# Performance work log

Measured on AMD Instinct MI355X. Metric: run time of the kernel, lower is better.

Reference implementation:

```python
import jax, jax.numpy as jnp
import numpy as np

BIT = 128
Y_P = 0.5
RIGHT = BIT / 8.0
LEFT = RIGHT / 2.0
UB = BIT / 2.0
ALPHA = 0.1
PCT_NUM, PCT_DEN = 9, 10  # percent = 9/10
C_COEF = (1.0 / RIGHT) * np.log(Y_P / (99.0 * (1.0 - Y_P)))  # slope c (constant since y_p fixed)
A_COEF = -1.0 / (LEFT * C_COEF) * np.log(99.0 * Y_P / (1.0 - Y_P))  # hard-branch factor a
# with y_p=0.5: d = -c*BP, g = -a*c*BP, so f_easy = c*(x-BP), f_hard = a*c*(x-BP)


def setup_inputs() -> dict:
    key = jax.random.key(0)
    k1, k2 = jax.random.split(key)
    N, C = 6144, 200
    u = jax.random.normal(k1, (N, BIT), dtype=jnp.float32)
    labels = jax.random.randint(k2, (N,), 0, C)
    y = jax.nn.one_hot(labels, C, dtype=jnp.int32)
    ind = jnp.arange(N, dtype=jnp.int32)  # unused dataset indices
    return {"u": u, "y": y, "ind": ind}


def reference(u, y, ind):
    sg = jax.lax.stop_gradient
    N = u.shape[0]
    uh = jnp.tanh(u)
    s = (y @ y.T) > 0                      # [N,N] bool similarity (diagonal is True)
    inner = uh @ uh.T                      # [N,N]
    n_sim = s.sum(axis=1)                  # int per-row similar count
    n_dis = N - n_sim
    fn_sim = n_sim.astype(jnp.float32)
    fn_dis = n_dis.astype(jnp.float32)
    idx = jnp.arange(N)[None, :]

    meanS = jnp.clip(jnp.where(s, inner, 0.0).sum(1) / jnp.maximum(fn_sim, 1.0), 0.0, UB)
    meanDS = jnp.clip(jnp.where(s, 0.0, inner).sum(1) / jnp.maximum(fn_dis, 1.0), 0.0, UB)

    dis_sorted = jnp.sort(jnp.where(s, -jnp.inf, inner), axis=1)
    start_dis = (n_dis * PCT_NUM) // PCT_DEN          # int(len*0.9)
    tail_mask = idx >= (N - n_dis + start_dis)[:, None]
    tail_cnt = jnp.maximum((n_dis - start_dis).astype(jnp.float32), 1.0)
    dMax = jnp.clip(jnp.where(tail_mask, dis_sorted, 0.0).sum(1) / tail_cnt, 0.0, UB)

    sim_sorted = jnp.sort(jnp.where(s, inner, jnp.inf), axis=1)
    start_sim = (n_sim * PCT_NUM) // PCT_DEN
    head_mask = idx < (n_sim - start_sim)[:, None]
    head_cnt = jnp.maximum((n_sim - start_sim).astype(jnp.float32), 1.0)
    sMin = jnp.clip(jnp.where(head_mask, sim_sorted, 0.0).sum(1) / head_cnt, 0.0, UB)

    # .item() in the original detaches these -> stop_gradient
    meanS, meanDS, dMax, sMin = map(sg, (meanS, meanDS, dMax, sMin))
    BP = meanS - (UB - meanS) / UB * jnp.abs(meanS - dMax)      # [N]
    BPd = meanDS + meanDS / UB * jnp.abs(meanDS - sMin)         # [N]

    # similar-pair loss: f + log(1+exp(-f)) == softplus(f)
    dc = inner - BP[:, None]
    f_sim = jnp.where(inner > BP[:, None], C_COEF * dc, A_COEF * C_COEF * dc)
    mask_sim = s & (inner != BP[:, None])             # == BP excluded in torch indexing
    cnt_sim = jnp.maximum(mask_sim.sum(1).astype(jnp.float32), 1.0)
    row_pos = jnp.where(mask_sim, jax.nn.softplus(f_sim), 0.0).sum(1) / cnt_sim

    # dissimilar-pair loss: log(1+exp(-f)) == softplus(-f)
    dcd = inner - BPd[:, None]
    f_dis = jnp.where(inner < BPd[:, None], C_COEF * dcd, A_COEF * C_COEF * dcd)
    mask_dis = (~s) & (inner != BPd[:, None])
    cnt_dis = jnp.maximum(mask_dis.sum(1).astype(jnp.float32), 1.0)
    row_neg = jnp.where(mask_dis, jax.nn.softplus(-f_dis), 0.0).sum(1) / cnt_dis

    valid = (n_sim > 0) & (n_dis > 0)
    count = valid.sum().astype(jnp.float32)
    posL = jnp.where(count > 0, jnp.where(valid, row_pos, 0.0).sum() / jnp.maximum(count, 1.0), 0.0)
    navL = jnp.where(count > 0, jnp.where(valid, row_neg, 0.0).sum() / jnp.maximum(count, 1.0), 0.0)

    q_loss = ALPHA * jnp.mean((uh - jnp.sign(uh)) ** 2)
    return posL + navL + q_loss
```

## Files before the change

kernel.cpp:

```cpp
#include <hip/hip_runtime.h>
#include <cstdint>

#define NROW 6144
#define KDIM 128
#define NLAB 200
#define C_COEF (-0.28719499063341177f)
#define UBV 64.0f

typedef _Float16 f16x8 __attribute__((ext_vector_type(8)));
typedef _Float16 f16x2 __attribute__((ext_vector_type(2)));
typedef float f32x4 __attribute__((ext_vector_type(4)));
typedef __attribute__((address_space(1))) const void as1c_void;
typedef __attribute__((address_space(3))) void as3_void;

union U8 { f16x8 h; unsigned u[4]; f16x2 p[4]; };
union CV16 { _Float16 h; unsigned short us; };

__device__ __forceinline__ float softplus_f(float x){
  return fmaxf(x, 0.f) + __logf(1.f + __expf(-fabsf(x)));
}
__device__ __forceinline__ float waveRedF(float v){
#pragma unroll
  for (int o = 32; o; o >>= 1) v += __shfl_down(v, o, 64);
  return v;
}
__device__ __forceinline__ float bfRedF(float v){
#pragma unroll
  for (int o = 32; o; o >>= 1) v += __shfl_xor(v, o, 64);
  return v;
}
__device__ __forceinline__ int bfRedI(int v){
#pragma unroll
  for (int o = 32; o; o >>= 1) v += __shfl_xor(v, o, 64);
  return v;
}
__device__ __forceinline__ int bfMaxI(int v){
#pragma unroll
  for (int o = 32; o; o >>= 1){ int x = __shfl_xor(v, o, 64); v = v > x ? v : x; }
  return v;
}
__device__ __forceinline__ float bfMaxF(float v){
#pragma unroll
  for (int o = 32; o; o >>= 1) v = fmaxf(v, __shfl_xor(v, o, 64));
  return v;
}
__device__ __forceinline__ float val_of_key(unsigned key){
  unsigned bits = (key & 0x8000u) ? (key ^ 0x8000u) : (key ^ 0xFFFFu);
  CV16 cv; cv.us = (unsigned short)bits;
  return (float)cv.h;
}

__global__ __launch_bounds__(256) void k_labtanh(const int* __restrict__ y,
    unsigned char* __restrict__ lab, int* __restrict__ cnt, int* __restrict__ simIdx,
    const float* __restrict__ u, _Float16* __restrict__ uhswz, float* __restrict__ accf){
  const int bid = blockIdx.x;
  const int tid = threadIdx.x;
  const int NLB = NROW / 4;
  if (bid < NLB){
    const int lane = tid & 63;
    const int row = bid * 4 + (tid >> 6);
    if (lane < NLAB / 4){
      const int4 v = ((const int4*)(y + (size_t)row * NLAB))[lane];
      int t = -1;
      if (v.x != 0) t = 4 * lane;
      if (v.y != 0) t = 4 * lane + 1;
      if (v.z != 0) t = 4 * lane + 2;
      if (v.w != 0) t = 4 * lane + 3;
      if (t >= 0){
        lab[row] = (unsigned char)t;
        int p = atomicAdd(&cnt[t], 1);
        if (p < 512) simIdx[t * 512 + p] = row;
      }
    }
    return;
  }
  const int gid = (bid - NLB) * 256 + tid;
  const int row = gid >> 4;
  const int h = gid & 15;
  const int g = h ^ (row & 7);
  const float* sp = u + (size_t)row * KDIM + g * 8;
  float q = 0.f;
  f16x8 o;
#pragma unroll
  for (int t = 0; t < 8; t++){
    float x = sp[t];
    float e2 = __expf(2.f * x);
    float th = 1.f - 2.f * __builtin_amdgcn_rcpf(e2 + 1.f);
    float sg = (th > 0.f) ? 1.f : ((th < 0.f) ? -1.f : 0.f);
    float d = th - sg;
    q += d * d;
    o[t] = (_Float16)th;
  }
  *(f16x8*)(uhswz + (size_t)row * KDIM + h * 8) = o;
  q = waveRedF(q);
  __shared__ float qb[4];
  if ((tid & 63) == 0) qb[tid >> 6] = q;
  __syncthreads();
  if (tid == 0) atomicAdd(&accf[0], qb[0] + qb[1] + qb[2] + qb[3]);
}

__global__ __launch_bounds__(512) void k_mm(const _Float16* __restrict__ A,
    _Float16* __restrict__ out, int row0, int sym){
  int bi, bj;
  if (sym){
    int t = blockIdx.x;
    int b = 0, off = 0;
    while (t >= off + (48 - b)){ off += 48 - b; b++; }
    bi = b; bj = b + (t - off);
  } else {
    bi = blockIdx.y; bj = blockIdx.x;
  }
  __shared__ __align__(16) _Float16 SH[2 * 128 * KDIM];
  const int tid = threadIdx.x;
  const int wav = tid >> 6, lane = tid & 63;
  const bool diag = sym && (bi == bj);

  const char* Ag = (const char*)(A + (size_t)(row0 + bi * 128) * KDIM);
  const char* Bg = (const char*)(A + (size_t)(bj * 128) * KDIM);
  char* Asb = (char*)SH;
  char* Bsb = diag ? Asb : (char*)(SH + 128 * KDIM);
#pragma unroll
  for (int t = 0; t < 4; t++){
    const int ub = wav * 4096 + t * 1024;
    __builtin_amdgcn_global_load_lds((as1c_void*)(Ag + ub + lane * 16),
                                     (as3_void*)(Asb + ub), 16, 0, 0);
    if (!diag)
      __builtin_amdgcn_global_load_lds((as1c_void*)(Bg + ub + lane * 16),
                                       (as3_void*)(Bsb + ub), 16, 0, 0);
  }
  __syncthreads();

  const int quad = lane >> 4, l16 = lane & 15;
  const int wm = (wav >> 2) * 64, wn = (wav & 3) * 32;
  f32x4 acc[4][2];
#pragma unroll
  for (int im = 0; im < 4; im++)
#pragma unroll
    for (int in = 0; in < 2; in++)
      acc[im][in] = (f32x4){0.f, 0.f, 0.f, 0.f};

#pragma unroll
  for (int kb = 0; kb < 4; kb++){
    f16x8 af[4], bf[2];
    const int gidx = kb * 4 + quad;
#pragma unroll
    for (int i = 0; i < 4; i++){
      const int m = wm + i * 16 + l16;
      af[i] = *(const f16x8*)(Asb + m * 256 + ((gidx ^ (m & 7)) << 4));
    }
#pragma unroll
    for (int j = 0; j < 2; j++){
      const int n = wn + j * 16 + l16;
      bf[j] = *(const f16x8*)(Bsb + n * 256 + ((gidx ^ (n & 7)) << 4));
    }
#pragma unroll
    for (int im = 0; im < 4; im++)
#pragma unroll
      for (int in = 0; in < 2; in++)
        acc[im][in] = __builtin_amdgcn_mfma_f32_16x16x32_f16(af[im], bf[in], acc[im][in], 0, 0, 0);
  }
  __syncthreads();

  _Float16* Cs = (_Float16*)SH;
#pragma unroll
  for (int im = 0; im < 4; im++)
#pragma unroll
    for (int in = 0; in < 2; in++)
#pragma unroll
      for (int r = 0; r < 4; r++){
        const int rl = wm + im * 16 + quad * 4 + r;
        const int cl = wn + in * 16 + l16;
        Cs[rl * 132 + cl] = (_Float16)acc[im][in][r];
      }
  __syncthreads();

  _Float16* obase = out + (size_t)(bi * 128) * NROW + (size_t)bj * 128;
  const int s = tid & 15;
  const int rb = tid >> 4;
#pragma unroll
  for (int i = 0; i < 4; i++){
    const int r = rb + i * 32;
    f16x8 vv = *(const f16x8*)(Cs + r * 132 + s * 8);
    *(f16x8*)(obase + (size_t)r * NROW + s * 8) = vv;
  }

  if (sym && bi != bj){
    __syncthreads();
#pragma unroll
    for (int im = 0; im < 4; im++)
#pragma unroll
      for (int in = 0; in < 2; in++)
#pragma unroll
        for (int r = 0; r < 4; r++){
          const int rl = wm + im * 16 + quad * 4 + r;
          const int cl = wn + in * 16 + l16;
          Cs[cl * 132 + rl] = (_Float16)acc[im][in][r];
        }
    __syncthreads();
    _Float16* obase2 = out + (size_t)(bj * 128) * NROW + (size_t)bi * 128;
#pragma unroll
    for (int i = 0; i < 4; i++){
      const int r = rb + i * 32;
      f16x8 vv = *(const f16x8*)(Cs + r * 132 + s * 8);
      *(f16x8*)(obase2 + (size_t)r * NROW + s * 8) = vv;
    }
  }
}

__global__ __launch_bounds__(256) void k_stats(const _Float16* __restrict__ buf,
    const unsigned char* __restrict__ lab, const int* __restrict__ cnt,
    const int* __restrict__ simIdx, float* __restrict__ rowRes, int row0){
  __shared__ int   histS[4][1028];
  __shared__ float simvS[4][512];
  const int tid = threadIdx.x;
  const int lane = tid & 63;
  const int wav = tid >> 6;
  const int lrow = blockIdx.x * 4 + wav;
  const int row = row0 + lrow;
  const int myl = lab[row];
  const int n_sim = cnt[myl];
  const int n_dis = NROW - n_sim;
  if (n_dis == 0 || n_sim == 0) return;
  const int k1 = n_dis - (n_dis * 9) / 10;
  const int k2 = n_sim - (n_sim * 9) / 10;
  const int ns = (n_sim < 512) ? n_sim : 512;

  int*   hist = histS[wav];
  int*   myh  = hist + (lane >> 4) * 257;
  float* simv = simvS[wav];
#pragma unroll
  for (int r = 0; r < 4; r++) *(int4*)&hist[(lane + 64 * r) * 4] = make_int4(0, 0, 0, 0);
  if (lane == 0) *(int4*)&hist[1024] = make_int4(0, 0, 0, 0);

  const f16x8* src = (const f16x8*)(buf + (size_t)lrow * NROW);
  const _Float16* srcs = buf + (size_t)lrow * NROW;

  float sumAll = 0.f;
  const f16x2 ones = (f16x2){(_Float16)1.f, (_Float16)1.f};
#pragma unroll 2
  for (int it = 0; it < 12; ++it){
    U8 x; x.h = src[it * 64 + lane];
#pragma unroll
    for (int k = 0; k < 4; k++){
      unsigned wv = x.u[k];
      unsigned m = (wv >> 15) & 0x00010001u;
      unsigned key2 = wv ^ 0x80008000u ^ (m * 0x7FFFu);
      atomicAdd(&myh[(key2 >> 8) & 0xFFu], 1);
      atomicAdd(&myh[key2 >> 24], 1);
#if __has_builtin(__builtin_amdgcn_fdot2)
      sumAll = __builtin_amdgcn_fdot2(x.p[k], ones, sumAll, false);
#else
      sumAll += (float)x.h[2 * k] + (float)x.h[2 * k + 1];
#endif
    }
  }

  float sumS = 0.f;
  for (int t = lane; t < ns; t += 64){
    int idx = simIdx[myl * 512 + t];
    CV16 cv; cv.h = srcs[idx];
    unsigned bits = (unsigned)cv.us;
    unsigned key = bits ^ 0x8000u ^ ((bits >> 15) * 0x7FFFu);
    float v = (float)cv.h;
    simv[t] = v; sumS += v;
    atomicAdd(&myh[key >> 8], -1);
  }
  sumAll = bfRedF(sumAll);
  sumS = bfRedF(sumS);
  const float sumD = sumAll - sumS;

  int cArr[4];
#pragma unroll
  for (int d = 0; d < 4; d++){
    const int b = 4 * lane + d;
    cArr[d] = hist[b] + hist[257 + b] + hist[514 + b] + hist[771 + b];
  }
  int part = cArr[0] + cArr[1] + cArr[2] + cArr[3];
  int suf = part;
#pragma unroll
  for (int o = 1; o < 64; o <<= 1){
    int x = __shfl_down(suf, o, 64);
    if (lane + o < 64) suf += x;
  }
  int cum = suf - part;
  int encB = -1, krF = 0;
#pragma unroll
  for (int d = 3; d >= 0; --d){
    int cd = cArr[d];
    if (k1 > cum && k1 <= cum + cd){ encB = 4 * lane + d; krF = k1 - cum; }
    cum += cd;
  }
  const int hbStar = bfMaxI(encB);
  const int kr1 = bfMaxI(krF);

#pragma unroll
  for (int r = 0; r < 4; r++) *(int4*)&hist[(lane + 64 * r) * 4] = make_int4(0, 0, 0, 0);
  if (lane == 0) *(int4*)&hist[1024] = make_int4(0, 0, 0, 0);

  float sAb = 0.f;
#pragma unroll 2
  for (int it = 0; it < 12; ++it){
    U8 x; x.h = src[it * 64 + lane];
#pragma unroll
    for (int k = 0; k < 4; k++){
      unsigned wv = x.u[k];
      unsigned m = (wv >> 15) & 0x00010001u;
      unsigned key2 = wv ^ 0x80008000u ^ (m * 0x7FFFu);
      int hbLo = (key2 >> 8) & 0xFF;
      int hbHi = key2 >> 24;
      if (hbLo > hbStar) sAb += (float)x.h[2 * k];
      else if (hbLo == hbStar) atomicAdd(&myh[key2 & 0xFFu], 1);
      if (hbHi > hbStar) sAb += (float)x.h[2 * k + 1];
      else if (hbHi == hbStar) atomicAdd(&myh[(key2 >> 16) & 0xFFu], 1);
    }
  }
  for (int t = lane; t < ns; t += 64){
    float v = simv[t];
    CV16 cv; cv.h = (_Float16)v;
    unsigned bits = (unsigned)cv.us;
    unsigned key = bits ^ 0x8000u ^ ((bits >> 15) * 0x7FFFu);
    int hb = (int)(key >> 8);
    if (hb > hbStar) sAb -= v;
    else if (hb == hbStar) atomicAdd(&myh[key & 0xFFu], -1);
  }
  sAb = bfRedF(sAb);

  int c2[4];
#pragma unroll
  for (int d = 0; d < 4; d++){
    const int b = 4 * lane + d;
    c2[d] = hist[b] + hist[257 + b] + hist[514 + b] + hist[771 + b];
  }
  part = c2[0] + c2[1] + c2[2] + c2[3];
  suf = part;
#pragma unroll
  for (int o = 1; o < 64; o <<= 1){
    int x = __shfl_down(suf, o, 64);
    if (lane + o < 64) suf += x;
  }
  cum = suf - part;
  int encL = -1, g2F = 0;
#pragma unroll
  for (int d = 3; d >= 0; --d){
    int cd = c2[d];
    if (kr1 > cum && kr1 <= cum + cd){ encL = 4 * lane + d; g2F = cum; }
    cum += cd;
  }
  const int lbStar = bfMaxI(encL);
  const int gt2 = bfMaxI(g2F);
  float sumIn = 0.f;
#pragma unroll
  for (int d = 0; d < 4; d++){
    int lb = 4 * lane + d;
    if (lb > lbStar) sumIn += (float)c2[d] * val_of_key((unsigned)((hbStar << 8) | lb));
  }
  sumIn = bfRedF(sumIn);
  const float piv = val_of_key((unsigned)((hbStar << 8) | lbStar));
  const float dSum = sAb + sumIn + (float)(kr1 - gt2) * piv;

  float fpiv2 = -3e38f; int flt = 0;
  for (int t = lane; t < ns; t += 64){
    float vt = simv[t];
    int lt = 0, eq = 0;
    for (int j = 0; j < ns; j++){
      float vj = simv[j];
      lt += (vj < vt); eq += (vj == vt);
    }
    if (lt < k2 && k2 <= lt + eq){ fpiv2 = vt; flt = lt; }
  }
  const float piv2 = bfMaxF(fpiv2);
  const int ltS = bfMaxI(flt);
  float slt = 0.f;
  for (int t = lane; t < ns; t += 64){
    float v = simv[t];
    if (v < piv2) slt += v;
  }
  slt = bfRedF(slt);
  const float sSum = slt + (float)(k2 - ltS) * piv2;

  const float meanS  = fminf(fmaxf(sumS / fmaxf((float)n_sim, 1.f), 0.f), UBV);
  const float meanDS = fminf(fmaxf(sumD / fmaxf((float)n_dis, 1.f), 0.f), UBV);
  const float dMax   = fminf(fmaxf(dSum / fmaxf((float)k1, 1.f), 0.f), UBV);
  const float sMin   = fminf(fmaxf(sSum / fmaxf((float)k2, 1.f), 0.f), UBV);
  const float BP  = meanS - (UBV - meanS) / UBV * fabsf(meanS - dMax);
  const float BPd = meanDS + meanDS / UBV * fabsf(meanDS - sMin);

  float an = 0.f; int ties = 0;
#pragma unroll 2
  for (int it = 0; it < 12; ++it){
    f16x8 h8 = src[it * 64 + lane];
#pragma unroll
    for (int e = 0; e < 8; e++){
      float v = (float)h8[e];
      float dcd = v - BPd;
      float f = ((dcd < 0.f) ? C_COEF : 2.f * C_COEF) * dcd;
      an += softplus_f(-f);
      ties += (dcd == 0.f);
    }
  }
  float spSim = 0.f; int tiesSim = 0;
  float ap = 0.f, cp = 0.f;
  for (int t = lane; t < ns; t += 64){
    float v = simv[t];
    float dcd = v - BPd;
    if (dcd == 0.f) tiesSim++;
    else {
      float f = ((dcd < 0.f) ? C_COEF : 2.f * C_COEF) * dcd;
      spSim += softplus_f(-f);
    }
    if (v != BP){
      float dc = v - BP;
      float f = (v > BP) ? C_COEF * dc : (2.f * C_COEF) * dc;
      ap += softplus_f(f); cp += 1.f;
    }
  }
  an = bfRedF(an); spSim = bfRedF(spSim);
  const int tiesT = bfRedI(ties);
  const int tiesSimT = bfRedI(tiesSim);
  ap = bfRedF(ap); cp = bfRedF(cp);
  if (lane == 0){
    const float L = __logf(1.f + __expf(-0.f));
    float anF = an - (float)tiesT * L - spSim;
    float cnF = (float)(n_dis - (tiesT - tiesSimT));
    float4 r;
    r.x = ap / fmaxf(cp, 1.f);
    r.y = anF / fmaxf(cnF, 1.f);
    r.z = 1.f;
    r.w = 0.f;
    *(float4*)(rowRes + 4 * (size_t)row) = r;
  }
}

__global__ __launch_bounds__(256) void k_final(const float* __restrict__ accf,
    const float* __restrict__ rowRes, float* __restrict__ out){
  const int tid = threadIdx.x;
  float p = 0.f, n = 0.f, c = 0.f;
  for (int i = tid; i < NROW; i += 256){
    float4 r = *(const float4*)(rowRes + 4 * (size_t)i);
    p += r.x; n += r.y; c += r.z;
  }
  p = bfRedF(p); n = bfRedF(n); c = bfRedF(c);
  __shared__ float sb[12];
  const int wav = tid >> 6;
  if ((tid & 63) == 0){ sb[wav] = p; sb[4 + wav] = n; sb[8 + wav] = c; }
  __syncthreads();
  if (tid == 0){
    p = sb[0] + sb[1] + sb[2] + sb[3];
    n = sb[4] + sb[5] + sb[6] + sb[7];
    c = sb[8] + sb[9] + sb[10] + sb[11];
    float posL = 0.f, navL = 0.f;
    if (c > 0.f){ posL = p / c; navL = n / c; }
    out[0] = posL + navL + 0.1f * (accf[0] / (float)(NROW * KDIM));
  }
}

extern "C" void kernel_launch(void* const* d_in, const int* in_sizes, int n_in,
                              void* d_out, int out_size, void* d_ws, size_t ws_size,
                              hipStream_t stream){
  const float* u = (const float*)d_in[0];
  const int* y = (const int*)d_in[1];
  char* ws = (char*)d_ws;
  float* accf = (float*)ws;
  int* cnt = (int*)(ws + 64);
  float* rowRes = (float*)(ws + 4096);
  unsigned char* lab = (unsigned char*)(ws + 102400);
  int* simIdx = (int*)(ws + 108544);
  _Float16* uhswz = (_Float16*)(ws + 518144);
  const size_t ibufOff = 518144 + (size_t)NROW * KDIM * 2;
  _Float16* ibuf = (_Float16*)(ws + ibufOff);

  hipMemsetAsync(d_ws, 0, 102400, stream);
  k_labtanh<<<NROW / 4 + (NROW * 16) / 256, 256, 0, stream>>>(y, lab, cnt, simIdx,
                                                              u, uhswz, accf);

  size_t avail = (ws_size > ibufOff) ? ws_size - ibufOff : 0;
  long maxRows = (long)(avail / ((size_t)NROW * 2));
  maxRows = (maxRows / 128) * 128;
  if (maxRows > NROW) maxRows = NROW;
  if (maxRows < 128) maxRows = 128;

  for (int r0 = 0; r0 < NROW; r0 += (int)maxRows){
    int rows = NROW - r0;
    if (rows > maxRows) rows = (int)maxRows;
    if (rows == NROW){
      k_mm<<<dim3(48 * 49 / 2), 512, 0, stream>>>(uhswz, ibuf, r0, 1);
    } else {
      k_mm<<<dim3(48, rows / 128), 512, 0, stream>>>(uhswz, ibuf, r0, 0);
    }
    k_stats<<<rows / 4, 256, 0, stream>>>(ibuf, lab, cnt, simIdx, rowRes, r0);
  }
  k_final<<<1, 256, 0, stream>>>(accf, rowRes, (float*)d_out);
}
```

Measured before the change: 165.1 us.

## Halve k_mm LDS via two K-phases, remap tiles, fold label pass into tanh

The GEMM kernel now stages A and B tiles in two K-halves of 64 columns each. This shrinks shared memory from 64KB to about 33KB so more blocks can be resident per CU, at the cost of an extra barrier pair per half. The symmetric triangular tile index is permuted with a stride of 147 so that consecutive blocks spread across the triangle. The label one-hot scan is merged into the tanh blocks, removing 1536 extra blocks. k_stats is now launched as two half-size grids over the row range via a new sub-row offset.

New measurement: 180.8 us. 9.5% more time.

```diff
diff --git a/kernel.cpp b/kernel.cpp
--- a/kernel.cpp
+++ b/kernel.cpp
@@ -55,11 +55,12 @@
     const float* __restrict__ u, _Float16* __restrict__ uhswz, float* __restrict__ accf){
   const int bid = blockIdx.x;
   const int tid = threadIdx.x;
-  const int NLB = NROW / 4;
-  if (bid < NLB){
-    const int lane = tid & 63;
-    const int row = bid * 4 + (tid >> 6);
-    if (lane < NLAB / 4){
+  const int lane = tid & 63, wav = tid >> 6;
+
+  if (lane < NLAB / 4){
+#pragma unroll
+    for (int j = 0; j < 4; j++){
+      const int row = bid * 16 + wav * 4 + j;
       const int4 v = ((const int4*)(y + (size_t)row * NLAB))[lane];
       int t = -1;
       if (v.x != 0) t = 4 * lane;
@@ -72,9 +73,9 @@
         if (p < 512) simIdx[t * 512 + p] = row;
       }
     }
-    return;
-  }
-  const int gid = (bid - NLB) * 256 + tid;
+  }
+
+  const int gid = bid * 256 + tid;
   const int row = gid >> 4;
   const int h = gid & 15;
   const int g = h ^ (row & 7);
@@ -104,64 +105,63 @@
   int bi, bj;
   if (sym){
     int t = blockIdx.x;
+    t = (t & 7) * 147 + (t >> 3);
     int b = 0, off = 0;
     while (t >= off + (48 - b)){ off += 48 - b; b++; }
     bi = b; bj = b + (t - off);
-  } else {
-    bi = blockIdx.y; bj = blockIdx.x;
-  }
-  __shared__ __align__(16) _Float16 SH[2 * 128 * KDIM];
+  } else { bi = blockIdx.y; bj = blockIdx.x; }
+  __shared__ __align__(16) _Float16 SH[128 * 132];
   const int tid = threadIdx.x;
   const int wav = tid >> 6, lane = tid & 63;
   const bool diag = sym && (bi == bj);
-
+  char* Asb = (char*)SH;
+  char* Bsb = diag ? Asb : (Asb + 16384);
   const char* Ag = (const char*)(A + (size_t)(row0 + bi * 128) * KDIM);
   const char* Bg = (const char*)(A + (size_t)(bj * 128) * KDIM);
-  char* Asb = (char*)SH;
-  char* Bsb = diag ? Asb : (char*)(SH + 128 * KDIM);
-#pragma unroll
-  for (int t = 0; t < 4; t++){
-    const int ub = wav * 4096 + t * 1024;
-    __builtin_amdgcn_global_load_lds((as1c_void*)(Ag + ub + lane * 16),
-                                     (as3_void*)(Asb + ub), 16, 0, 0);
-    if (!diag)
-      __builtin_amdgcn_global_load_lds((as1c_void*)(Bg + ub + lane * 16),
-                                       (as3_void*)(Bsb + ub), 16, 0, 0);
-  }
-  __syncthreads();
-
   const int quad = lane >> 4, l16 = lane & 15;
   const int wm = (wav >> 2) * 64, wn = (wav & 3) * 32;
+  const int grow0 = lane >> 3;
+  const int gcol = (lane & 7) * 16;
+
   f32x4 acc[4][2];
 #pragma unroll
-  for (int im = 0; im < 4; im++)
-#pragma unroll
-    for (int in = 0; in < 2; in++)
-      acc[im][in] = (f32x4){0.f, 0.f, 0.f, 0.f};
-
-#pragma unroll
-  for (int kb = 0; kb < 4; kb++){
-    f16x8 af[4], bf[2];
-    const int gidx = kb * 4 + quad;
-#pragma unroll
-    for (int i = 0; i < 4; i++){
-      const int m = wm + i * 16 + l16;
-      af[i] = *(const f16x8*)(Asb + m * 256 + ((gidx ^ (m & 7)) << 4));
-    }
-#pragma unroll
-    for (int j = 0; j < 2; j++){
-      const int n = wn + j * 16 + l16;
-      bf[j] = *(const f16x8*)(Bsb + n * 256 + ((gidx ^ (n & 7)) << 4));
-    }
-#pragma unroll
-    for (int im = 0; im < 4; im++)
-#pragma unroll
-      for (int in = 0; in < 2; in++)
-        acc[im][in] = __builtin_amdgcn_mfma_f32_16x16x32_f16(af[im], bf[in], acc[im][in], 0, 0, 0);
-  }
-  __syncthreads();
-
-  _Float16* Cs = (_Float16*)SH;
+  for (int i = 0; i < 4; i++)
+#pragma unroll
+    for (int j = 0; j < 2; j++)
+      acc[i][j] = (f32x4){0.f, 0.f, 0.f, 0.f};
+
+#pragma unroll
+  for (int half = 0; half < 2; ++half){
+#pragma unroll
+    for (int t2 = 0; t2 < 2; t2++){
+      const int base = (wav * 2 + t2) * 1024;
+      const int grow = (base >> 7) + grow0;
+      const size_t goff = (size_t)grow * 256 + half * 128 + gcol;
+      __builtin_amdgcn_global_load_lds((as1c_void*)(Ag + goff),
+                                       (as3_void*)(Asb + base + lane * 16), 16, 0, 0);
+      if (!diag)
+        __builtin_amdgcn_global_load_lds((as1c_void*)(Bg + goff),
+                                         (as3_void*)(Bsb + base + lane * 16), 16, 0, 0);
+    }
+    __syncthreads();
+#pragma unroll
+    for (int kb = 0; kb < 2; kb++){
+      const int gl = kb * 4 + quad;
+      const int n0 = wn + l16, n1 = wn + 16 + l16;
+      f16x8 bf0 = *(const f16x8*)(Bsb + n0 * 128 + ((gl ^ (n0 & 7)) << 4));
+      f16x8 bf1 = *(const f16x8*)(Bsb + n1 * 128 + ((gl ^ (n1 & 7)) << 4));
+#pragma unroll
+      for (int i = 0; i < 4; i++){
+        const int m = wm + i * 16 + l16;
+        f16x8 af = *(const f16x8*)(Asb + m * 128 + ((gl ^ (m & 7)) << 4));
+        acc[i][0] = __builtin_amdgcn_mfma_f32_16x16x32_f16(af, bf0, acc[i][0], 0, 0, 0);
+        acc[i][1] = __builtin_amdgcn_mfma_f32_16x16x32_f16(af, bf1, acc[i][1], 0, 0, 0);
+      }
+    }
+    __syncthreads();
+  }
+
+  _Float16* Cs = SH;
 #pragma unroll
   for (int im = 0; im < 4; im++)
 #pragma unroll
@@ -209,13 +209,13 @@
 
 __global__ __launch_bounds__(256) void k_stats(const _Float16* __restrict__ buf,
     const unsigned char* __restrict__ lab, const int* __restrict__ cnt,
-    const int* __restrict__ simIdx, float* __restrict__ rowRes, int row0){
+    const int* __restrict__ simIdx, float* __restrict__ rowRes, int row0, int sub0){
   __shared__ int   histS[4][1028];
   __shared__ float simvS[4][512];
   const int tid = threadIdx.x;
   const int lane = tid & 63;
   const int wav = tid >> 6;
-  const int lrow = blockIdx.x * 4 + wav;
+  const int lrow = sub0 + blockIdx.x * 4 + wav;
   const int row = row0 + lrow;
   const int myl = lab[row];
   const int n_sim = cnt[myl];
@@ -470,8 +470,8 @@
   _Float16* ibuf = (_Float16*)(ws + ibufOff);
 
   hipMemsetAsync(d_ws, 0, 102400, stream);
-  k_labtanh<<<NROW / 4 + (NROW * 16) / 256, 256, 0, stream>>>(y, lab, cnt, simIdx,
-                                                              u, uhswz, accf);
+  k_labtanh<<<(NROW * 16) / 256, 256, 0, stream>>>(y, lab, cnt, simIdx,
+                                                   u, uhswz, accf);
 
   size_t avail = (ws_size > ibufOff) ? ws_size - ibufOff : 0;
   long maxRows = (long)(avail / ((size_t)NROW * 2));
@@ -487,7 +487,9 @@
     } else {
       k_mm<<<dim3(48, rows / 128), 512, 0, stream>>>(uhswz, ibuf, r0, 0);
     }
-    k_stats<<<rows / 4, 256, 0, stream>>>(ibuf, lab, cnt, simIdx, rowRes, r0);
+    const int h1 = (rows / 8) * 4;
+    k_stats<<<h1 / 4, 256, 0, stream>>>(ibuf, lab, cnt, simIdx, rowRes, r0, 0);
+    k_stats<<<(rows - h1) / 4, 256, 0, stream>>>(ibuf, lab, cnt, simIdx, rowRes, r0, h1);
   }
   k_final<<<1, 256, 0, stream>>>(accf, rowRes, (float*)d_out);
 }
```

## Use single per-wave histogram in stats kernel and split its launch

Applied to the files above, without the earlier changes.

Drops the four lane-group sub-histograms in k_stats and uses one 257-bin histogram per wave. This cuts LDS use per block and turns the bin readout into a single int4 load. The catch is more atomic contention within a wave. The stats launch is also split into two half-size launches with a row offset, and the workspace memset shrinks to the first 4096 bytes. The split launch adds launch overhead with no clear benefit, and the smaller memset relies on rowRes not needing zeroing.

New measurement: 179.6 us. 1.09x slower.

```diff
diff --git a/kernel.cpp b/kernel.cpp
--- a/kernel.cpp
+++ b/kernel.cpp
@@ -161,7 +161,7 @@
   }
   __syncthreads();
 
-  _Float16* Cs = (_Float16*)SH;
+  _Float16* Cs = SH;
 #pragma unroll
   for (int im = 0; im < 4; im++)
 #pragma unroll
@@ -209,13 +209,13 @@
 
 __global__ __launch_bounds__(256) void k_stats(const _Float16* __restrict__ buf,
     const unsigned char* __restrict__ lab, const int* __restrict__ cnt,
-    const int* __restrict__ simIdx, float* __restrict__ rowRes, int row0){
-  __shared__ int   histS[4][1028];
+    const int* __restrict__ simIdx, float* __restrict__ rowRes, int row0, int sub0){
+  __shared__ int   histS[4][260];
   __shared__ float simvS[4][512];
   const int tid = threadIdx.x;
   const int lane = tid & 63;
   const int wav = tid >> 6;
-  const int lrow = blockIdx.x * 4 + wav;
+  const int lrow = sub0 + blockIdx.x * 4 + wav;
   const int row = row0 + lrow;
   const int myl = lab[row];
   const int n_sim = cnt[myl];
@@ -226,11 +226,9 @@
   const int ns = (n_sim < 512) ? n_sim : 512;
 
   int*   hist = histS[wav];
-  int*   myh  = hist + (lane >> 4) * 257;
   float* simv = simvS[wav];
-#pragma unroll
-  for (int r = 0; r < 4; r++) *(int4*)&hist[(lane + 64 * r) * 4] = make_int4(0, 0, 0, 0);
-  if (lane == 0) *(int4*)&hist[1024] = make_int4(0, 0, 0, 0);
+  *(int4*)&hist[lane * 4] = make_int4(0, 0, 0, 0);
+  if (lane == 0) hist[256] = 0;
 
   const f16x8* src = (const f16x8*)(buf + (size_t)lrow * NROW);
   const _Float16* srcs = buf + (size_t)lrow * NROW;
@@ -245,8 +243,8 @@
       unsigned wv = x.u[k];
       unsigned m = (wv >> 15) & 0x00010001u;
       unsigned key2 = wv ^ 0x80008000u ^ (m * 0x7FFFu);
-      atomicAdd(&myh[(key2 >> 8) & 0xFFu], 1);
-      atomicAdd(&myh[key2 >> 24], 1);
+      atomicAdd(&hist[(key2 >> 8) & 0xFFu], 1);
+      atomicAdd(&hist[key2 >> 24], 1);
 #if __has_builtin(__builtin_amdgcn_fdot2)
       sumAll = __builtin_amdgcn_fdot2(x.p[k], ones, sumAll, false);
 #else
@@ -263,18 +261,15 @@
     unsigned key = bits ^ 0x8000u ^ ((bits >> 15) * 0x7FFFu);
     float v = (float)cv.h;
     simv[t] = v; sumS += v;
-    atomicAdd(&myh[key >> 8], -1);
+    atomicAdd(&hist[key >> 8], -1);
   }
   sumAll = bfRedF(sumAll);
   sumS = bfRedF(sumS);
   const float sumD = sumAll - sumS;
 
   int cArr[4];
-#pragma unroll
-  for (int d = 0; d < 4; d++){
-    const int b = 4 * lane + d;
-    cArr[d] = hist[b] + hist[257 + b] + hist[514 + b] + hist[771 + b];
-  }
+  { int4 c4 = *(const int4*)&hist[4 * lane];
+    cArr[0] = c4.x; cArr[1] = c4.y; cArr[2] = c4.z; cArr[3] = c4.w; }
   int part = cArr[0] + cArr[1] + cArr[2] + cArr[3];
   int suf = part;
 #pragma unroll
@@ -293,9 +288,8 @@
   const int hbStar = bfMaxI(encB);
   const int kr1 = bfMaxI(krF);
 
-#pragma unroll
-  for (int r = 0; r < 4; r++) *(int4*)&hist[(lane + 64 * r) * 4] = make_int4(0, 0, 0, 0);
-  if (lane == 0) *(int4*)&hist[1024] = make_int4(0, 0, 0, 0);
+  *(int4*)&hist[lane * 4] = make_int4(0, 0, 0, 0);
+  if (lane == 0) hist[256] = 0;
 
   float sAb = 0.f;
 #pragma unroll 2
@@ -309,9 +303,9 @@
       int hbLo = (key2 >> 8) & 0xFF;
       int hbHi = key2 >> 24;
       if (hbLo > hbStar) sAb += (float)x.h[2 * k];
-      else if (hbLo == hbStar) atomicAdd(&myh[key2 & 0xFFu], 1);
+      else if (hbLo == hbStar) atomicAdd(&hist[key2 & 0xFFu], 1);
       if (hbHi > hbStar) sAb += (float)x.h[2 * k + 1];
-      else if (hbHi == hbStar) atomicAdd(&myh[(key2 >> 16) & 0xFFu], 1);
+      else if (hbHi == hbStar) atomicAdd(&hist[(key2 >> 16) & 0xFFu], 1);
     }
   }
   for (int t = lane; t < ns; t += 64){
@@ -321,16 +315,13 @@
     unsigned key = bits ^ 0x8000u ^ ((bits >> 15) * 0x7FFFu);
     int hb = (int)(key >> 8);
     if (hb > hbStar) sAb -= v;
-    else if (hb == hbStar) atomicAdd(&myh[key & 0xFFu], -1);
+    else if (hb == hbStar) atomicAdd(&hist[key & 0xFFu], -1);
   }
   sAb = bfRedF(sAb);
 
   int c2[4];
-#pragma unroll
-  for (int d = 0; d < 4; d++){
-    const int b = 4 * lane + d;
-    c2[d] = hist[b] + hist[257 + b] + hist[514 + b] + hist[771 + b];
-  }
+  { int4 c4 = *(const int4*)&hist[4 * lane];
+    c2[0] = c4.x; c2[1] = c4.y; c2[2] = c4.z; c2[3] = c4.w; }
   part = c2[0] + c2[1] + c2[2] + c2[3];
   suf = part;
 #pragma unroll
@@ -469,7 +460,7 @@
   const size_t ibufOff = 518144 + (size_t)NROW * KDIM * 2;
   _Float16* ibuf = (_Float16*)(ws + ibufOff);
 
-  hipMemsetAsync(d_ws, 0, 102400, stream);
+  hipMemsetAsync(d_ws, 0, 4096, stream);
   k_labtanh<<<NROW / 4 + (NROW * 16) / 256, 256, 0, stream>>>(y, lab, cnt, simIdx,
                                                               u, uhswz, accf);
 
@@ -487,7 +478,9 @@
     } else {
       k_mm<<<dim3(48, rows / 128), 512, 0, stream>>>(uhswz, ibuf, r0, 0);
     }
-    k_stats<<<rows / 4, 256, 0, stream>>>(ibuf, lab, cnt, simIdx, rowRes, r0);
+    const int h1 = (rows / 8) * 4;
+    k_stats<<<h1 / 4, 256, 0, stream>>>(ibuf, lab, cnt, simIdx, rowRes, r0, 0);
+    k_stats<<<(rows - h1) / 4, 256, 0, stream>>>(ibuf, lab, cnt, simIdx, rowRes, r0, h1);
   }
   k_final<<<1, 256, 0, stream>>>(accf, rowRes, (float*)d_out);
 }
```
